# Kernel optimization log

Hardware: AMD Instinct MI355X
Metric: run time of the kernel (lower is better)

Reference implementation:

```python
import jax, jax.numpy as jnp
import numpy as np

N_NODES = 4096
IN_FEAT = 256
N_HEADS = 8
N_HIDDEN = 64  # out_features // n_heads
NEG_SLOPE = 0.2
EDGE_PROB = 0.05


def setup_inputs() -> dict:
    key = jax.random.key(0)
    k1, k2, k3, k4 = jax.random.split(key, 4)
    h = jax.random.normal(k1, (N_NODES, IN_FEAT), dtype=jnp.float32)
    # binary adjacency mask [N, N, 1] (broadcast over heads), as in the torch asserts
    adj_mat = (jax.random.uniform(k2, (N_NODES, N_NODES, 1)) < EDGE_PROB).astype(jnp.float32)
    # nn.Linear(in_features, n_heads*n_hidden, bias=False) weight: [H*F, in]
    W = jax.random.normal(k3, (N_HEADS * N_HIDDEN, IN_FEAT), dtype=jnp.float32) / np.sqrt(IN_FEAT)
    # nn.Linear(2*n_hidden, 1, bias=False) weight, flattened: [2*F]
    a = jax.random.normal(k4, (2 * N_HIDDEN,), dtype=jnp.float32) / np.sqrt(2 * N_HIDDEN)
    return {"h": h, "adj_mat": adj_mat, "W": W, "a": a}


def reference(h, adj_mat, W, a):
    n = h.shape[0]
    # g: [N, H, F]
    g = (h @ W.T).reshape(n, N_HEADS, N_HIDDEN)
    # attn(cat[g_i, g_j]) == a_l . g_i + a_r . g_j  (linear, no bias)
    a_l = a[:N_HIDDEN]
    a_r = a[N_HIDDEN:]
    el = jnp.einsum('ihf,f->ih', g, a_l)  # [N, H]
    er = jnp.einsum('jhf,f->jh', g, a_r)  # [N, H]
    e = jax.nn.leaky_relu(el[:, None, :] + er[None, :, :], NEG_SLOPE)  # [N, N, H]
    # note: original multiplies scores by adjacency (not masked_fill)
    e = e * adj_mat  # adj broadcasts over heads
    att = jax.nn.softmax(e, axis=1)  # softmax over source nodes j
    # dropout is identity at eval (dropout_rate=0.0)
    out = jnp.einsum('ijh,jhf->ihf', att, g)  # [N, H, F]
    return out.reshape(n, N_HEADS * N_HIDDEN)
```

## Files before the change

kernel.cpp:

```cpp
#include <hip/hip_runtime.h>

#define N_NODES 4096
#define IN_FEAT 256
#define N_HEADS 8
#define N_HIDDEN 64
#define OUT_FEAT (N_HEADS * N_HIDDEN)
#define NEG_SLOPE 0.2f

typedef _Float16 half8 __attribute__((ext_vector_type(8)));
typedef _Float16 h2 __attribute__((ext_vector_type(2)));
typedef float floatx4 __attribute__((ext_vector_type(4)));
typedef float floatx16 __attribute__((ext_vector_type(16)));
typedef float f4 __attribute__((ext_vector_type(4)));

__global__ __launch_bounds__(256) void produce(
    const float* __restrict__ H, const float* __restrict__ adj,
    const float* __restrict__ Wt, const float* __restrict__ a,
    _Float16* __restrict__ GT16, float* __restrict__ elT,
    _Float16* __restrict__ eR1h, _Float16* __restrict__ eR2h,
    unsigned long long* __restrict__ bits) {
  __shared__ _Float16 SM[4 * 64 * 64];
  const int t = threadIdx.x;
  const int bx = blockIdx.x, by = blockIdx.y;

  if (by >= 8) {
    const int c = bx * 8 + (by - 8);
    const size_t W0 = (size_t)c * 512;
    const int wv = t >> 6, lane = t & 63;
    for (int k0 = 0; k0 < 128; k0 += 8) {
      float v[8];
#pragma unroll
      for (int k = 0; k < 8; ++k)
        v[k] = adj[(W0 + wv * 128 + k0 + k) * 64 + lane];
#pragma unroll
      for (int k = 0; k < 8; ++k) {
        unsigned long long m = __ballot(v[k] != 0.f);
        if (lane == 0) bits[W0 + wv * 128 + k0 + k] = m;
      }
    }
    return;
  }

  _Float16* Ah = SM;
  _Float16* Al = SM + 4096;
  _Float16* Bh = SM + 8192;
  _Float16* Bl = SM + 12288;
  const int w = t >> 6, l = t & 63;
  const int n16 = l & 15, q = l >> 4;
  const int bi = bx, bo = by;
  const int m0 = bi * 64 + w * 16;

  floatx4 acc[4];
#pragma unroll
  for (int ct = 0; ct < 4; ++ct) acc[ct] = (floatx4)0.f;

  for (int kc = 0; kc < 4; ++kc) {
    if (kc) __syncthreads();
#pragma unroll
    for (int p = 0; p < 4; ++p) {
      const int idx = p * 256 + t;
      const int r = idx >> 4;
      const int c4 = (idx & 15) << 2;
      const int dst = r * 64 + ((((idx & 15) >> 1)) ^ (r & 7)) * 8 + (idx & 1) * 4;
      float4 hv = *(const float4*)(H + (size_t)(bi * 64 + r) * IN_FEAT + kc * 64 + c4);
      float4 wv = *(const float4*)(Wt + (size_t)(bo * 64 + r) * IN_FEAT + kc * 64 + c4);
      union { _Float16 h[4]; int2 d; } hh_, hl_, wh_, wl_;
      hh_.h[0] = (_Float16)hv.x; hh_.h[1] = (_Float16)hv.y;
      hh_.h[2] = (_Float16)hv.z; hh_.h[3] = (_Float16)hv.w;
      hl_.h[0] = (_Float16)(hv.x - (float)hh_.h[0]);
      hl_.h[1] = (_Float16)(hv.y - (float)hh_.h[1]);
      hl_.h[2] = (_Float16)(hv.z - (float)hh_.h[2]);
      hl_.h[3] = (_Float16)(hv.w - (float)hh_.h[3]);
      wh_.h[0] = (_Float16)wv.x; wh_.h[1] = (_Float16)wv.y;
      wh_.h[2] = (_Float16)wv.z; wh_.h[3] = (_Float16)wv.w;
      wl_.h[0] = (_Float16)(wv.x - (float)wh_.h[0]);
      wl_.h[1] = (_Float16)(wv.y - (float)wh_.h[1]);
      wl_.h[2] = (_Float16)(wv.z - (float)wh_.h[2]);
      wl_.h[3] = (_Float16)(wv.w - (float)wh_.h[3]);
      *(int2*)&Ah[dst] = hh_.d;
      *(int2*)&Al[dst] = hl_.d;
      *(int2*)&Bh[dst] = wh_.d;
      *(int2*)&Bl[dst] = wl_.d;
    }
    __syncthreads();
#pragma unroll
    for (int ks = 0; ks < 2; ++ks) {
      const int ao = (w * 16 + n16) * 64 + (((ks << 2) + q) ^ (n16 & 7)) * 8;
      half8 Afh = *(const half8*)&Ah[ao];
      half8 Afl = *(const half8*)&Al[ao];
#pragma unroll
      for (int ct = 0; ct < 4; ++ct) {
        const int bofs = (ct * 16 + n16) * 64 + (((ks << 2) + q) ^ (n16 & 7)) * 8;
        half8 Bfh = *(const half8*)&Bh[bofs];
        half8 Bfl = *(const half8*)&Bl[bofs];
        acc[ct] = __builtin_amdgcn_mfma_f32_16x16x32_f16(Afh, Bfh, acc[ct], 0, 0, 0);
        acc[ct] = __builtin_amdgcn_mfma_f32_16x16x32_f16(Afl, Bfh, acc[ct], 0, 0, 0);
        acc[ct] = __builtin_amdgcn_mfma_f32_16x16x32_f16(Afh, Bfl, acc[ct], 0, 0, 0);
      }
    }
  }

  float aLv[4], aRv[4];
#pragma unroll
  for (int ct = 0; ct < 4; ++ct) {
    aLv[ct] = a[ct * 16 + n16];
    aRv[ct] = a[64 + ct * 16 + n16];
  }
#pragma unroll
  for (int reg = 0; reg < 4; ++reg) {
    float sl = 0.f, sr = 0.f;
#pragma unroll
    for (int ct = 0; ct < 4; ++ct) {
      sl = fmaf(acc[ct][reg], aLv[ct], sl);
      sr = fmaf(acc[ct][reg], aRv[ct], sr);
    }
#pragma unroll
    for (int off = 1; off < 16; off <<= 1) {
      sl += __shfl_xor(sl, off);
      sr += __shfl_xor(sr, off);
    }
    if (n16 == 0) {
      const int rowi = m0 + q * 4 + reg;
      elT[(size_t)bo * N_NODES + rowi] = sl;
      eR1h[(size_t)bo * N_NODES + rowi] = (_Float16)__expf(sr);
      eR2h[(size_t)bo * N_NODES + rowi] = (_Float16)__expf(0.2f * sr);
    }
  }

  __syncthreads();
  _Float16* LG = SM;
#pragma unroll
  for (int ct = 0; ct < 4; ++ct)
#pragma unroll
    for (int reg = 0; reg < 4; ++reg)
      LG[(w * 16 + q * 4 + reg) * 72 + ct * 16 + n16] = (_Float16)acc[ct][reg];
  __syncthreads();
  {
    const int f = t >> 2, jq = t & 3;
    union { _Float16 hh[16]; int4 v[2]; } u;
#pragma unroll
    for (int k = 0; k < 16; ++k) u.hh[k] = LG[(jq * 16 + k) * 72 + f];
    _Float16* dst = GT16 + (size_t)(bo * 64 + f) * N_NODES + bi * 64 + jq * 16;
    *(int4*)dst = u.v[0];
    *(int4*)(dst + 8) = u.v[1];
  }
}

__global__ __launch_bounds__(256, 4) void attn_v9(
    const unsigned long long* __restrict__ bits, const _Float16* __restrict__ GT16,
    const float* __restrict__ elT, const _Float16* __restrict__ eR1h,
    const _Float16* __restrict__ eR2h, float* __restrict__ out) {
  __shared__ __align__(16) _Float16 Gt[2][4][2048];
  __shared__ float eL1s[32], eL2s[32];
  __shared__ float Zp[4][32];

  const int t = threadIdx.x;
  const int ib = blockIdx.x, h = blockIdx.y;
  const int i0 = ib * 32;
  const int w = t >> 6, l = t & 63;
  const int c31 = l & 31, hi = l >> 5, hi8 = hi * 8;

  const _Float16* gsrcs[4];
#pragma unroll
  for (int c = 0; c < 4; ++c) {
    const int feat = c * 16 + (l >> 2);
    const int p = l & 3;
    gsrcs[c] = GT16 + (size_t)(h * 64 + feat) * N_NODES + w * 1024 + (p ^ (feat & 3)) * 8;
  }

  const _Float16* er1p = eR1h + (size_t)h * N_NODES + w * 1024 + hi8;
  const _Float16* er2p = eR2h + (size_t)h * N_NODES + w * 1024 + hi8;
  const unsigned* bp = (const unsigned*)bits + (size_t)(i0 + c31) * 128 + w * 32;

  if (t < 32) {
    float e = elT[(size_t)h * N_NODES + i0 + t];
    eL1s[t] = __expf(e);
    eL2s[t] = __expf(0.2f * e);
  }

#pragma unroll
  for (int c = 0; c < 4; ++c)
    __builtin_amdgcn_global_load_lds(
        (const __attribute__((address_space(1))) unsigned int*)gsrcs[c],
        (__attribute__((address_space(3))) unsigned int*)&Gt[0][w][c * 512],
        16, 0, 0);
  uint4 e1c0 = *(const uint4*)er1p;
  uint4 e1c1 = *(const uint4*)(er1p + 16);
  uint4 e2c0 = *(const uint4*)er2p;
  uint4 e2c1 = *(const uint4*)(er2p + 16);
  unsigned bvc = bp[0];
  __syncthreads();

  const _Float16 e1f = (_Float16)eL1s[c31];
  const _Float16 e2f = (_Float16)eL2s[c31];
  const h2 eL1h2 = {e1f, e1f};
  const h2 eL2h2 = {e2f, e2f};
  half8 Bones;
#pragma unroll
  for (int k = 0; k < 8; ++k) Bones[k] = (c31 == 0) ? (_Float16)1.f : (_Float16)0.f;

  int boff[2][2];
#pragma unroll
  for (int ft = 0; ft < 2; ++ft)
#pragma unroll
    for (int ch = 0; ch < 2; ++ch)
      boff[ft][ch] = (ft * 32 + c31) * 32 + (((ch * 2 + hi) ^ (c31 & 3)) * 8);

  floatx16 acc0 = (floatx16)0.f, acc1 = (floatx16)0.f, accZ = (floatx16)0.f;

  int par = 0;
  for (int step = 0; step < 32; ++step) {
    uint4 e1n0 = e1c0, e1n1 = e1c1, e2n0 = e2c0, e2n1 = e2c1;
    unsigned bvn = bvc;
    if (step + 1 < 32) {
      const int np = par ^ 1;
#pragma unroll
      for (int c = 0; c < 4; ++c)
        __builtin_amdgcn_global_load_lds(
            (const __attribute__((address_space(1))) unsigned int*)(gsrcs[c] + (step + 1) * 32),
            (__attribute__((address_space(3))) unsigned int*)&Gt[np][w][c * 512],
            16, 0, 0);
      e1n0 = *(const uint4*)(er1p + (step + 1) * 32);
      e1n1 = *(const uint4*)(er1p + (step + 1) * 32 + 16);
      e2n0 = *(const uint4*)(er2p + (step + 1) * 32);
      e2n1 = *(const uint4*)(er2p + (step + 1) * 32 + 16);
      bvn = bp[step + 1];
    }
    const _Float16* gt = &Gt[par][w][0];
#pragma unroll
    for (int ch = 0; ch < 2; ++ch) {
      const unsigned byte = (bvc >> (ch * 16 + hi8)) & 0xffu;
      const uint4 r1 = ch ? e1c1 : e1c0;
      const uint4 r2 = ch ? e2c1 : e2c0;
      const unsigned r1a[4] = {r1.x, r1.y, r1.z, r1.w};
      const unsigned r2a[4] = {r2.x, r2.y, r2.z, r2.w};
      unsigned pr[4];
#pragma unroll
      for (int kk = 0; kk < 4; ++kk) {
        h2 pa = eL1h2 * __builtin_bit_cast(h2, r1a[kk]);
        h2 pb = eL2h2 * __builtin_bit_cast(h2, r2a[kk]);
        h2 pv = __builtin_elementwise_max(pa, pb);
        unsigned y = (byte >> (2 * kk)) & 3u;
        unsigned b01 = (y | (y << 15)) & 0x00010001u;
        unsigned keep = b01 * 0xffffu;
        pr[kk] = (__builtin_bit_cast(unsigned, pv) & keep) | (0x3C003C00u & ~keep);
      }
      const uint4 prv = {pr[0], pr[1], pr[2], pr[3]};
      half8 Af = __builtin_bit_cast(half8, prv);
      half8 B0 = *(const half8*)&gt[boff[0][ch]];
      half8 B1 = *(const half8*)&gt[boff[1][ch]];
      acc0 = __builtin_amdgcn_mfma_f32_32x32x16_f16(Af, B0, acc0, 0, 0, 0);
      acc1 = __builtin_amdgcn_mfma_f32_32x32x16_f16(Af, B1, acc1, 0, 0, 0);
      accZ = __builtin_amdgcn_mfma_f32_32x32x16_f16(Af, Bones, accZ, 0, 0, 0);
    }
    e1c0 = e1n0; e1c1 = e1n1; e2c0 = e2n0; e2c1 = e2n1; bvc = bvn;
    __syncthreads();
    par ^= 1;
  }

  float* sc = (float*)&Gt[0][0][0];
#pragma unroll
  for (int ft = 0; ft < 2; ++ft) {
#pragma unroll
    for (int r = 0; r < 16; ++r) {
      const int row = (r & 3) + 8 * (r >> 2) + 4 * hi;
      const int col = (ft * 32 + c31 + row * 4) & 63;
      sc[w * 2048 + row * 64 + col] = ft ? acc1[r] : acc0[r];
    }
  }
  if (c31 == 0) {
#pragma unroll
    for (int r = 0; r < 16; ++r)
      Zp[w][(r & 3) + 8 * (r >> 2) + 4 * hi] = accZ[r];
  }
  __syncthreads();
  {
    const int row = t >> 3, cg = (t & 7) * 8;
    const int sA = (cg + row * 4) & 63;
    const int sB = (cg + 4 + row * 4) & 63;
    f4 s0 = (f4)0.f, s1 = (f4)0.f;
#pragma unroll
    for (int w4 = 0; w4 < 4; ++w4) {
      s0 += *(const f4*)&sc[w4 * 2048 + row * 64 + sA];
      s1 += *(const f4*)&sc[w4 * 2048 + row * 64 + sB];
    }
    const float Z = Zp[0][row] + Zp[1][row] + Zp[2][row] + Zp[3][row];
    const float invz = 1.f / Z;
    s0 *= invz;
    s1 *= invz;
    float* op = out + (size_t)(i0 + row) * OUT_FEAT + h * 64 + cg;
    *(f4*)op = s0;
    *(f4*)(op + 4) = s1;
  }
}

extern "C" void kernel_launch(void* const* d_in, const int* in_sizes, int n_in,
                              void* d_out, int out_size, void* d_ws, size_t ws_size,
                              hipStream_t stream) {
  const float* h   = (const float*)d_in[0];
  const float* adj = (const float*)d_in[1];
  const float* W   = (const float*)d_in[2];
  const float* a   = (const float*)d_in[3];
  float* out = (float*)d_out;

  char* ws = (char*)d_ws;
  _Float16* GT16 = (_Float16*)ws;
  unsigned long long* bits = (unsigned long long*)(ws + 4u * 1024 * 1024);
  float* elT = (float*)(ws + 6u * 1024 * 1024);
  _Float16* eR1h = (_Float16*)(ws + 6u * 1024 * 1024 + 128 * 1024);
  _Float16* eR2h = (_Float16*)(ws + 6u * 1024 * 1024 + 192 * 1024);

  produce<<<dim3(64, 16), 256, 0, stream>>>(h, adj, W, a, GT16, elT, eR1h, eR2h, bits);
  attn_v9<<<dim3(128, 8), 256, 0, stream>>>(bits, GT16, elT, eR1h, eR2h, out);
}
```

Before: 173.4 us.

## Restructure attention j-tiling to 64-wide chunks with shared eR staging in LDS

Changes the attention kernel's work split from four warps each owning a 1024-node slice of j to two j-halves with paired warps covering a 64-column chunk per step. eR1/eR2 factors are now staged once per block in double-buffered LDS by a few threads instead of loaded per lane from global memory, and the adjacency bits are read as 64-bit words. The LDS tile layout and XOR swizzle move to 8 segments. The intent is fewer redundant global loads and wider contiguous G loads. The cost is extra LDS traffic and dropping the occupancy hint from launch_bounds.

```diff
diff --git a/kernel.cpp b/kernel.cpp
--- a/kernel.cpp
+++ b/kernel.cpp
@@ -146,11 +146,13 @@
   }
 }
 
-__global__ __launch_bounds__(256, 4) void attn_v9(
+__global__ __launch_bounds__(256) void attn_v17(
     const unsigned long long* __restrict__ bits, const _Float16* __restrict__ GT16,
     const float* __restrict__ elT, const _Float16* __restrict__ eR1h,
     const _Float16* __restrict__ eR2h, float* __restrict__ out) {
-  __shared__ __align__(16) _Float16 Gt[2][4][2048];
+  __shared__ __align__(16) _Float16 Gt[2][2][4096];
+  __shared__ __align__(16) _Float16 eRs1[2][2][64];
+  __shared__ __align__(16) _Float16 eRs2[2][2][64];
   __shared__ float eL1s[32], eL2s[32];
   __shared__ float Zp[4][32];
 
@@ -158,37 +160,41 @@
   const int ib = blockIdx.x, h = blockIdx.y;
   const int i0 = ib * 32;
   const int w = t >> 6, l = t & 63;
-  const int c31 = l & 31, hi = l >> 5, hi8 = hi * 8;
+  const int c31 = l & 31, hi = l >> 5;
+  const int jh = w >> 1, jsub = w & 1;
 
   const _Float16* gsrcs[4];
+  int ldsbase[4];
 #pragma unroll
   for (int c = 0; c < 4; ++c) {
-    const int feat = c * 16 + (l >> 2);
-    const int p = l & 3;
-    gsrcs[c] = GT16 + (size_t)(h * 64 + feat) * N_NODES + w * 1024 + (p ^ (feat & 3)) * 8;
-  }
-
-  const _Float16* er1p = eR1h + (size_t)h * N_NODES + w * 1024 + hi8;
-  const _Float16* er2p = eR2h + (size_t)h * N_NODES + w * 1024 + hi8;
-  const unsigned* bp = (const unsigned*)bits + (size_t)(i0 + c31) * 128 + w * 32;
+    const int flat = w * 256 + c * 64 + l;
+    const int fjh = flat >> 9;
+    const int ff = (flat >> 3) & 63;
+    const int ss = flat & 7;
+    const int cg = ss ^ (ff & 7);
+    gsrcs[c] = GT16 + (size_t)(h * 64 + ff) * N_NODES + fjh * 2048 + cg * 8;
+    ldsbase[c] = (w * 256 + c * 64) * 8;
+  }
+  const int era = (t >> 3) & 1, erjh = t >> 4, erseg = t & 7;
+  const _Float16* esrc0 = (era ? eR2h : eR1h) + (size_t)h * N_NODES + erjh * 2048 + erseg * 8;
+  const unsigned long long* bp = bits + (size_t)(i0 + c31) * 64 + jh * 32;
 
   if (t < 32) {
     float e = elT[(size_t)h * N_NODES + i0 + t];
     eL1s[t] = __expf(e);
     eL2s[t] = __expf(0.2f * e);
   }
-
 #pragma unroll
   for (int c = 0; c < 4; ++c)
     __builtin_amdgcn_global_load_lds(
         (const __attribute__((address_space(1))) unsigned int*)gsrcs[c],
-        (__attribute__((address_space(3))) unsigned int*)&Gt[0][w][c * 512],
+        (__attribute__((address_space(3))) unsigned int*)(&Gt[0][0][0] + ldsbase[c]),
         16, 0, 0);
-  uint4 e1c0 = *(const uint4*)er1p;
-  uint4 e1c1 = *(const uint4*)(er1p + 16);
-  uint4 e2c0 = *(const uint4*)er2p;
-  uint4 e2c1 = *(const uint4*)(er2p + 16);
-  unsigned bvc = bp[0];
+  if (t < 32) {
+    int4 ev = *(const int4*)esrc0;
+    *(int4*)&(era ? eRs2 : eRs1)[0][erjh][erseg * 8] = ev;
+  }
+  unsigned long long bvc = bp[0];
   __syncthreads();
 
   const _Float16 e1f = (_Float16)eL1s[c31];
@@ -199,39 +205,30 @@
 #pragma unroll
   for (int k = 0; k < 8; ++k) Bones[k] = (c31 == 0) ? (_Float16)1.f : (_Float16)0.f;
 
-  int boff[2][2];
-#pragma unroll
-  for (int ft = 0; ft < 2; ++ft)
-#pragma unroll
-    for (int ch = 0; ch < 2; ++ch)
-      boff[ft][ch] = (ft * 32 + c31) * 32 + (((ch * 2 + hi) ^ (c31 & 3)) * 8);
-
   floatx16 acc0 = (floatx16)0.f, acc1 = (floatx16)0.f, accZ = (floatx16)0.f;
 
   int par = 0;
   for (int step = 0; step < 32; ++step) {
-    uint4 e1n0 = e1c0, e1n1 = e1c1, e2n0 = e2c0, e2n1 = e2c1;
-    unsigned bvn = bvc;
+    int4 ev;
+    unsigned long long bvn = bvc;
     if (step + 1 < 32) {
       const int np = par ^ 1;
 #pragma unroll
       for (int c = 0; c < 4; ++c)
         __builtin_amdgcn_global_load_lds(
-            (const __attribute__((address_space(1))) unsigned int*)(gsrcs[c] + (step + 1) * 32),
-            (__attribute__((address_space(3))) unsigned int*)&Gt[np][w][c * 512],
+            (const __attribute__((address_space(1))) unsigned int*)(gsrcs[c] + (step + 1) * 64),
+            (__attribute__((address_space(3))) unsigned int*)(&Gt[np][0][0] + ldsbase[c]),
             16, 0, 0);
-      e1n0 = *(const uint4*)(er1p + (step + 1) * 32);
-      e1n1 = *(const uint4*)(er1p + (step + 1) * 32 + 16);
-      e2n0 = *(const uint4*)(er2p + (step + 1) * 32);
-      e2n1 = *(const uint4*)(er2p + (step + 1) * 32 + 16);
+      if (t < 32) ev = *(const int4*)(esrc0 + (step + 1) * 64);
       bvn = bp[step + 1];
     }
-    const _Float16* gt = &Gt[par][w][0];
-#pragma unroll
-    for (int ch = 0; ch < 2; ++ch) {
-      const unsigned byte = (bvc >> (ch * 16 + hi8)) & 0xffu;
-      const uint4 r1 = ch ? e1c1 : e1c0;
-      const uint4 r2 = ch ? e2c1 : e2c0;
+    const _Float16* gt = &Gt[par][jh][0];
+#pragma unroll
+    for (int ks = 0; ks < 2; ++ks) {
+      const int sl = jsub * 4 + ks * 2 + hi;
+      const unsigned byte = (unsigned)(bvc >> (sl * 8)) & 0xffu;
+      uint4 r1 = *(const uint4*)&eRs1[par][jh][sl * 8];
+      uint4 r2 = *(const uint4*)&eRs2[par][jh][sl * 8];
       const unsigned r1a[4] = {r1.x, r1.y, r1.z, r1.w};
       const unsigned r2a[4] = {r2.x, r2.y, r2.z, r2.w};
       unsigned pr[4];
@@ -247,13 +244,16 @@
       }
       const uint4 prv = {pr[0], pr[1], pr[2], pr[3]};
       half8 Af = __builtin_bit_cast(half8, prv);
-      half8 B0 = *(const half8*)&gt[boff[0][ch]];
-      half8 B1 = *(const half8*)&gt[boff[1][ch]];
+      const int sp = (sl ^ (c31 & 7)) * 8;
+      half8 B0 = *(const half8*)&gt[(c31)*64 + sp];
+      half8 B1 = *(const half8*)&gt[(32 + c31) * 64 + sp];
       acc0 = __builtin_amdgcn_mfma_f32_32x32x16_f16(Af, B0, acc0, 0, 0, 0);
       acc1 = __builtin_amdgcn_mfma_f32_32x32x16_f16(Af, B1, acc1, 0, 0, 0);
       accZ = __builtin_amdgcn_mfma_f32_32x32x16_f16(Af, Bones, accZ, 0, 0, 0);
     }
-    e1c0 = e1n0; e1c1 = e1n1; e2c0 = e2n0; e2c1 = e2n1; bvc = bvn;
+    if (step + 1 < 32 && t < 32)
+      *(int4*)&(era ? eRs2 : eRs1)[par ^ 1][erjh][erseg * 8] = ev;
+    bvc = bvn;
     __syncthreads();
     par ^= 1;
   }
@@ -311,5 +311,5 @@
   _Float16* eR2h = (_Float16*)(ws + 6u * 1024 * 1024 + 192 * 1024);
 
   produce<<<dim3(64, 16), 256, 0, stream>>>(h, adj, W, a, GT16, elT, eR1h, eR2h, bits);
-  attn_v9<<<dim3(128, 8), 256, 0, stream>>>(bits, GT16, elT, eR1h, eR2h, out);
+  attn_v17<<<dim3(128, 8), 256, 0, stream>>>(bits, GT16, elT, eR1h, eR2h, out);
 }
```

After: 173.4 us. Within noise of the previous version (+0.0%).
